# Performance work log

Hardware: AMD Instinct MI355X
Metric: run time of the kernel (lower is better)

Reference implementation:

```python
import jax, jax.numpy as jnp
import numpy as np

EPS = 1e-5
LEAK = 0.1
NPOINT = 4096
NSAMPLE = 32


def setup_inputs() -> dict:
    key = jax.random.key(0)
    ks = jax.random.split(key, 6)
    B, N, Cin = 2, 16384, 64
    ch = [Cin + 3, 64, 64, 128]
    xyz = jax.random.normal(ks[0], (B, 3, N), jnp.float32)
    points = jax.random.normal(ks[1], (B, Cin, N), jnp.float32)
    W0 = jax.random.normal(ks[2], (ch[1], ch[0]), jnp.float32) * 0.05
    W1 = jax.random.normal(ks[3], (ch[2], ch[1]), jnp.float32) * 0.05
    W2 = jax.random.normal(ks[4], (ch[3], ch[2]), jnp.float32) * 0.05
    return dict(
        xyz=xyz, points=points, W0=W0, W1=W1, W2=W2,
        g0=jnp.ones((ch[1],), jnp.float32), b0=jnp.zeros((ch[1],), jnp.float32),
        g1=jnp.ones((ch[2],), jnp.float32), b1=jnp.zeros((ch[2],), jnp.float32),
        g2=jnp.ones((ch[3],), jnp.float32), b2=jnp.zeros((ch[3],), jnp.float32),
    )


def _mlp_bn_act(x, W, g, b):
    # 1x1 conv (no bias) + BatchNorm2d (training: batch stats, biased var) + LeakyReLU(0.1)
    x = jnp.einsum('oc,bcsk->bosk', W, x)
    m = jnp.mean(x, axis=(0, 2, 3), keepdims=True)
    v = jnp.mean(jnp.square(x - m), axis=(0, 2, 3), keepdims=True)
    x = (x - m) * jax.lax.rsqrt(v + EPS) * g[None, :, None, None] + b[None, :, None, None]
    return jnp.where(x >= 0, x, LEAK * x)


def reference(xyz, points, W0, W1, W2, g0, b0, g1, b1, g2, b2):
    B, _, N = xyz.shape
    xyz_t = jnp.transpose(xyz, (0, 2, 1))            # [B,N,3]
    new_xyz = xyz[:, :, :NPOINT]                     # [B,3,S]  (use_fps=False path)
    new_xyz_t = jnp.transpose(new_xyz, (0, 2, 1))    # [B,S,3]

    # squared distances [B,S,N]
    d = (jnp.sum(new_xyz_t ** 2, -1)[:, :, None]
         + jnp.sum(xyz_t ** 2, -1)[:, None, :]
         - 2.0 * jnp.einsum('bsc,bnc->bsn', new_xyz_t, xyz_t))
    _, knn_idx = jax.lax.top_k(-d, NSAMPLE)          # [B,S,K] nearest neighbors

    gather = jax.vmap(lambda arr, idx: arr[idx])     # ([N,C],[S,K]) -> [S,K,C]
    neighbor_xyz = gather(xyz_t, knn_idx)            # [B,S,K,3]
    direction = neighbor_xyz - new_xyz_t[:, :, None, :]
    grouped = gather(jnp.transpose(points, (0, 2, 1)), knn_idx)  # [B,S,K,Cin]

    x = jnp.transpose(jnp.concatenate([direction, grouped], -1), (0, 3, 1, 2))  # [B,Cin+3,S,K]
    x = _mlp_bn_act(x, W0, g0, b0)
    x = _mlp_bn_act(x, W1, g1, b1)
    x = _mlp_bn_act(x, W2, g2, b2)
    new_points = jnp.max(x, axis=-1)                 # [B,128,S] max-pool over nsample
    return new_xyz, new_points
```

## Files before the change

kernel.cpp:

```cpp
#include <hip/hip_runtime.h>
#include <hip/hip_bf16.h>
#include <stdint.h>

#define N_ALL   16384
#define NPOINT  4096
#define KNN_K   32
#define BATCH   2
#define P_TOT   (BATCH*NPOINT*KNN_K)
#define P_TOTF  262144.0f
#define EPSV    1e-5f

typedef __attribute__((ext_vector_type(8))) short bf16x8;
typedef __attribute__((ext_vector_type(4))) float f32x4;

__device__ unsigned short g_knn[P_TOT];
__device__ __attribute__((aligned(16))) float g_pxyzn[BATCH*N_ALL*4];
__device__ __attribute__((aligned(16))) short g_ptb[BATCH*N_ALL*64];
__device__ __attribute__((aligned(16))) short g_x0b[(size_t)P_TOT*64];
__device__ __attribute__((aligned(16))) short g_x1b[(size_t)P_TOT*64];
__device__ __attribute__((aligned(16))) float g_mx[(size_t)BATCH*NPOINT*128];
__device__ __attribute__((aligned(16))) float g_mn[(size_t)BATCH*NPOINT*128];
__device__ __attribute__((aligned(16))) short g_Wb0[4*3*64*8];
__device__ __attribute__((aligned(16))) short g_Wb1[4*2*64*8];
__device__ __attribute__((aligned(16))) short g_Wb2[8*2*64*8];
__device__ float g_p0s[4][128];
__device__ float g_p1s[4][128];
__device__ float g_p2s[8][256];

__device__ __forceinline__ float b2f(short s) {
  union { unsigned u; float f; } v; v.u = ((unsigned)(unsigned short)s) << 16; return v.f;
}
__device__ __forceinline__ short f2b(float f) {
  union { float f; unsigned u; } v; v.f = f;
  unsigned u = v.u;
  u += 0x7FFFu + ((u >> 16) & 1u);
  return (short)(u >> 16);
}
__device__ __forceinline__ unsigned pkbf(float a, float b) {
  union { __hip_bfloat162 h; unsigned u; } v;
  v.h = __float22bfloat162_rn(make_float2(a, b));
  return v.u;
}
__device__ __forceinline__ unsigned long long bperm64(unsigned long long v, int byteaddr) {
  int lo = __builtin_amdgcn_ds_bpermute(byteaddr, (int)(unsigned)(v & 0xFFFFFFFFULL));
  int hi = __builtin_amdgcn_ds_bpermute(byteaddr, (int)(unsigned)(v >> 32));
  return (((unsigned long long)(unsigned)hi) << 32) | (unsigned)lo;
}
__device__ __forceinline__ unsigned long long u64min(unsigned long long a, unsigned long long b) {
  return a < b ? a : b;
}
__device__ __forceinline__ unsigned long long selstage(unsigned long long v,
                                                       unsigned long long pv, bool mx) {
  bool lt = v < pv;
  return (lt != mx) ? v : pv;
}

__device__ __forceinline__ void knn_merge32(unsigned long long& vL,
                                            unsigned long long& worst,
                                            unsigned& worst_hi, float& wd,
                                            unsigned long long vB, int hl,
                                            int aX1, int aX2, int aX4, int aX8,
                                            int aX16, int aRev, int aW) {
  vB = selstage(vB, bperm64(vB, aX1),  ((hl & 1) != 0) != ((hl & 2) != 0));
  vB = selstage(vB, bperm64(vB, aX2),  ((hl & 2) != 0) != ((hl & 4) != 0));
  vB = selstage(vB, bperm64(vB, aX1),  ((hl & 1) != 0) != ((hl & 4) != 0));
  vB = selstage(vB, bperm64(vB, aX4),  ((hl & 4) != 0) != ((hl & 8) != 0));
  vB = selstage(vB, bperm64(vB, aX2),  ((hl & 2) != 0) != ((hl & 8) != 0));
  vB = selstage(vB, bperm64(vB, aX1),  ((hl & 1) != 0) != ((hl & 8) != 0));
  vB = selstage(vB, bperm64(vB, aX8),  ((hl & 8) != 0) != ((hl & 16) != 0));
  vB = selstage(vB, bperm64(vB, aX4),  ((hl & 4) != 0) != ((hl & 16) != 0));
  vB = selstage(vB, bperm64(vB, aX2),  ((hl & 2) != 0) != ((hl & 16) != 0));
  vB = selstage(vB, bperm64(vB, aX1),  ((hl & 1) != 0) != ((hl & 16) != 0));
  vB = selstage(vB, bperm64(vB, aX16), (hl & 16) != 0);
  vB = selstage(vB, bperm64(vB, aX8),  (hl & 8) != 0);
  vB = selstage(vB, bperm64(vB, aX4),  (hl & 4) != 0);
  vB = selstage(vB, bperm64(vB, aX2),  (hl & 2) != 0);
  vB = selstage(vB, bperm64(vB, aX1),  (hl & 1) != 0);
  vL = u64min(vL, bperm64(vB, aRev));
  vL = selstage(vL, bperm64(vL, aX16), (hl & 16) != 0);
  vL = selstage(vL, bperm64(vL, aX8),  (hl & 8) != 0);
  vL = selstage(vL, bperm64(vL, aX4),  (hl & 4) != 0);
  vL = selstage(vL, bperm64(vL, aX2),  (hl & 2) != 0);
  vL = selstage(vL, bperm64(vL, aX1),  (hl & 1) != 0);
  worst = bperm64(vL, aW);
  worst_hi = (unsigned)(worst >> 32);
  unsigned wh = worst_hi;
  unsigned ub = (wh & 0x80000000u) ? (wh ^ 0x80000000u) : ~wh;
  wd = (wh == 0xFFFFFFFFu) ? __builtin_inff() : __uint_as_float(ub);
}

__global__ __launch_bounds__(256) void k_setup(const float* __restrict__ xyz,
                                               const float* __restrict__ points,
                                               const float* __restrict__ W0,
                                               const float* __restrict__ W1,
                                               const float* __restrict__ W2,
                                               float* __restrict__ out) {
#pragma clang fp contract(off)
  __shared__ float tile[64][65];
  int blk = blockIdx.x;
  int t = threadIdx.x;
  if (blk < 512) {
    int b  = blk >> 8;
    int n0 = (blk & 255) << 6;
#pragma unroll
    for (int r = 0; r < 16; r++) {
      int lin = r * 256 + t;
      int c = lin >> 6, nn = lin & 63;
      tile[c][nn] = points[((size_t)(b * 64 + c)) * N_ALL + n0 + nn];
    }
    __syncthreads();
#pragma unroll
    for (int r = 0; r < 16; r++) {
      int lin = r * 256 + t;
      int nn = lin >> 6, c = lin & 63;
      g_ptb[((size_t)(b * N_ALL + n0 + nn)) * 64 + c] = f2b(tile[c][nn]);
    }
  } else if (blk < 640) {
    int i = (blk - 512) * 256 + t;
    if (i < 24576) {
      int s = i & 4095;
      int c = (i >> 12) % 3;
      int b = i / 12288;
      out[i] = xyz[(b * 3 + c) * N_ALL + s];
    }
    int b = i >> 14, n = i & 16383;
    const float* xb = xyz + b * 3 * N_ALL;
    float x = xb[n], y = xb[N_ALL + n], z = xb[2 * N_ALL + n];
    float4 p; p.x = x; p.y = y; p.z = z; p.w = x * x + y * y + z * z;
    ((float4*)g_pxyzn)[i] = p;
  } else {
    for (int i = t; i < 4 * 3 * 64 * 8; i += 256) {
      int j = i & 7, lane = (i >> 3) & 63, rest = i >> 9;
      int kt = rest % 3, mt = rest / 3;
      int m = 16 * mt + (lane & 15);
      int k = 32 * kt + (lane >> 4) * 8 + j;
      float v = 0.f;
      if (k < 64) v = W0[m * 67 + 3 + k];
      else if (k < 67) v = W0[m * 67 + (k - 64)];
      g_Wb0[i] = f2b(v);
    }
    for (int i = t; i < 4 * 2 * 64 * 8; i += 256) {
      int j = i & 7, lane = (i >> 3) & 63;
      int kt = (i >> 9) & 1, mt = i >> 10;
      int m = 16 * mt + (lane & 15);
      int k = 32 * kt + (lane >> 4) * 8 + j;
      g_Wb1[i] = f2b(W1[m * 64 + k]);
    }
    for (int i = t; i < 8 * 2 * 64 * 8; i += 256) {
      int j = i & 7, lane = (i >> 3) & 63;
      int kt = (i >> 9) & 1, mt = i >> 10;
      int m = 16 * mt + (lane & 15);
      int k = 32 * kt + (lane >> 4) * 8 + j;
      g_Wb2[i] = f2b(W2[m * 64 + k]);
    }
    float* z0 = &g_p0s[0][0];
    float* z1 = &g_p1s[0][0];
    float* z2 = &g_p2s[0][0];
    for (int i = t; i < 512; i += 256) { z0[i] = 0.f; z1[i] = 0.f; }
    for (int i = t; i < 2048; i += 256) z2[i] = 0.f;
  }
}

__global__ __launch_bounds__(256, 8) void k_knn() {
#pragma clang fp contract(off)
  __shared__ unsigned long long buf[4][2][64];
  int wv = threadIdx.x >> 6;
  int lane = threadIdx.x & 63;
  int half = lane >> 5;
  int hl = lane & 31;
  int lanebase = lane & 32;
  unsigned long long* bufh = buf[wv][half];

  int qpair = wv >> 1;
  int range = wv & 1;
  int q = blockIdx.x * 4 + qpair * 2 + half;
  int b = q >> 12, s = q & 4095;
  const float4* pb = (const float4*)g_pxyzn + (b << 14);
  float4 qp = pb[s];
  float qx = qp.x, qy = qp.y, qz = qp.z, qn = qp.w;

  int aX1  = (lanebase | (hl ^ 1))  << 2;
  int aX2  = (lanebase | (hl ^ 2))  << 2;
  int aX4  = (lanebase | (hl ^ 4))  << 2;
  int aX8  = (lanebase | (hl ^ 8))  << 2;
  int aX16 = (lanebase | (hl ^ 16)) << 2;
  int aRev = (lanebase | (31 - hl)) << 2;
  int aW   = (lanebase | 31)        << 2;

  unsigned long long vL = ~0ULL;
  unsigned long long worst = ~0ULL;
  unsigned worst_hi = 0xFFFFFFFFu;
  float wd = __builtin_inff();
  int F = 0;

  int base = range << 13;
  for (int n0 = base; n0 < base + 8192; n0 += 128) {
    float4 p0 = pb[n0 + hl];
    float4 p1 = pb[n0 + 32 + hl];
    float4 p2 = pb[n0 + 64 + hl];
    float4 p3 = pb[n0 + 96 + hl];
    float d[4];
    {
      float dt0 = (qx * p0.x + qy * p0.y) + qz * p0.z;
      float dt1 = (qx * p1.x + qy * p1.y) + qz * p1.z;
      float dt2 = (qx * p2.x + qy * p2.y) + qz * p2.z;
      float dt3 = (qx * p3.x + qy * p3.y) + qz * p3.z;
      d[0] = __builtin_fmaf(-2.0f, dt0, qn + p0.w);
      d[1] = __builtin_fmaf(-2.0f, dt1, qn + p1.w);
      d[2] = __builtin_fmaf(-2.0f, dt2, qn + p2.w);
      d[3] = __builtin_fmaf(-2.0f, dt3, qn + p3.w);
    }
    float md = fminf(fminf(d[0], d[1]), fminf(d[2], d[3]));
    if (__ballot(md <= wd)) {
#pragma unroll
      for (int t = 0; t < 4; t++) {
        bool sv = d[t] <= wd;
        unsigned long long bl = __ballot(sv);
        unsigned mb = half ? (unsigned)(bl >> 32) : (unsigned)bl;
        if (sv) {
          unsigned u = __float_as_uint(d[t]);
          u ^= ((unsigned)(((int)u) >> 31)) | 0x80000000u;
          unsigned long long c = (((unsigned long long)u) << 32)
                               | (unsigned)(n0 + 32 * t + hl);
          bufh[F + __popc(mb & ((1u << hl) - 1u))] = c;
        }
        F += __popc(mb);
        if (__ballot(F >= 32)) {
          int take = F >= 32 ? 32 : F;
          unsigned long long vB = (hl < take) ? bufh[hl] : ~0ULL;
          knn_merge32(vL, worst, worst_hi, wd, vB, hl,
                      aX1, aX2, aX4, aX8, aX16, aRev, aW);
          int R = F - take;
          if (hl < R) bufh[hl] = bufh[32 + hl];
          F = R;
        }
      }
    }
  }
  if (__ballot(F > 0)) {
    unsigned long long vB = (hl < F) ? bufh[hl] : ~0ULL;
    knn_merge32(vL, worst, worst_hi, wd, vB, hl, aX1, aX2, aX4, aX8, aX16, aRev, aW);
  }

  bufh[hl] = vL;
  __syncthreads();
  unsigned long long vB = buf[wv ^ 1][half][hl];
  vL = u64min(vL, bperm64(vB, aRev));
  vL = selstage(vL, bperm64(vL, aX16), (hl & 16) != 0);
  vL = selstage(vL, bperm64(vL, aX8),  (hl & 8) != 0);
  vL = selstage(vL, bperm64(vL, aX4),  (hl & 4) != 0);
  vL = selstage(vL, bperm64(vL, aX2),  (hl & 2) != 0);
  vL = selstage(vL, bperm64(vL, aX1),  (hl & 1) != 0);
  if (range == 0)
    g_knn[((size_t)q << 5) | hl] = (unsigned short)(vL & 0xFFFF);
}

__global__ __launch_bounds__(256) void k_l0(const float* __restrict__ xyz) {
  __shared__ __attribute__((aligned(16))) short feats[256][104];
  int t = threadIdx.x;
  int p0 = blockIdx.x * 256;
  {
    int p = p0 + t;
    int idx = g_knn[p];
    int s = (p >> 5) & 4095;
    int b = p >> 17;
    const short* src = g_ptb + ((size_t)((b << 14) + idx) << 6);
#pragma unroll
    for (int i = 0; i < 8; i++)
      ((int4*)&feats[t][0])[i] = ((const int4*)src)[i];
    const float* xb = xyz + b * 3 * N_ALL;
    int4 z; z.x = 0; z.y = 0; z.z = 0; z.w = 0;
    *(int4*)&feats[t][64] = z;
    *(int4*)&feats[t][72] = z;
    *(int4*)&feats[t][80] = z;
    *(int4*)&feats[t][88] = z;
    short4 d3;
    d3.x = f2b(xb[idx] - xb[s]);
    d3.y = f2b(xb[N_ALL + idx] - xb[N_ALL + s]);
    d3.z = f2b(xb[2 * N_ALL + idx] - xb[2 * N_ALL + s]);
    d3.w = 0;
    *(short4*)&feats[t][64] = d3;
  }
  __syncthreads();
  int lane = t & 63, wv = t >> 6;
  int l15 = lane & 15, quad = lane >> 4;
  bf16x8 A[4][3];
#pragma unroll
  for (int mt = 0; mt < 4; mt++)
#pragma unroll
    for (int kt = 0; kt < 3; kt++)
      A[mt][kt] = *(const bf16x8*)(g_Wb0 + (((mt * 3 + kt) * 64 + lane) << 3));
  f32x4 C[4][4];
#pragma unroll
  for (int mt = 0; mt < 4; mt++)
#pragma unroll
    for (int nt = 0; nt < 4; nt++) C[mt][nt] = 0.f;
#pragma unroll
  for (int kt = 0; kt < 3; kt++)
#pragma unroll
    for (int nt = 0; nt < 4; nt++) {
      bf16x8 B = *(const bf16x8*)(&feats[wv * 64 + nt * 16 + l15][kt * 32 + quad * 8]);
#pragma unroll
      for (int mt = 0; mt < 4; mt++)
        C[mt][nt] = __builtin_amdgcn_mfma_f32_16x16x32_bf16(A[mt][kt], B, C[mt][nt], 0, 0, 0);
    }
  float sA[16], qA[16];
#pragma unroll
  for (int i = 0; i < 16; i++) { sA[i] = 0.f; qA[i] = 0.f; }
#pragma unroll
  for (int mt = 0; mt < 4; mt++)
#pragma unroll
    for (int nt = 0; nt < 4; nt++) {
      int p = p0 + wv * 64 + nt * 16 + l15;
      int c0 = mt * 16 + quad * 4;
      uint2 o;
      o.x = pkbf(C[mt][nt][0], C[mt][nt][1]);
      o.y = pkbf(C[mt][nt][2], C[mt][nt][3]);
      *(uint2*)(g_x0b + ((size_t)p << 6) + c0) = o;
      float v0 = __uint_as_float(o.x << 16);
      float v1 = __uint_as_float(o.x & 0xFFFF0000u);
      float v2 = __uint_as_float(o.y << 16);
      float v3 = __uint_as_float(o.y & 0xFFFF0000u);
      int ib = mt * 4;
      sA[ib+0] += v0; qA[ib+0] = fmaf(v0, v0, qA[ib+0]);
      sA[ib+1] += v1; qA[ib+1] = fmaf(v1, v1, qA[ib+1]);
      sA[ib+2] += v2; qA[ib+2] = fmaf(v2, v2, qA[ib+2]);
      sA[ib+3] += v3; qA[ib+3] = fmaf(v3, v3, qA[ib+3]);
    }
  __syncthreads();
  float* red = (float*)&feats[0][0];
  int rb = t * 36;
#pragma unroll
  for (int w = 0; w < 4; w++) {
    float4 vs; vs.x = sA[w*4+0]; vs.y = sA[w*4+1]; vs.z = sA[w*4+2]; vs.w = sA[w*4+3];
    float4 vq; vq.x = qA[w*4+0]; vq.y = qA[w*4+1]; vq.z = qA[w*4+2]; vq.w = qA[w*4+3];
    *(float4*)&red[rb + w*4] = vs;
    *(float4*)&red[rb + 16 + w*4] = vq;
  }
  __syncthreads();
  if (t < 64) {
    int qd = (t >> 2) & 3;
    int i = ((t >> 4) << 2) | (t & 3);
    float S = 0.f, Q = 0.f;
#pragma unroll
    for (int w = 0; w < 4; w++)
#pragma unroll
      for (int l = 0; l < 16; l++) {
        int row = (w * 64 + qd * 16 + l) * 36;
        S += red[row + i];
        Q += red[row + 16 + i];
      }
    float* sh = &g_p0s[blockIdx.x & 3][0];
    atomicAdd(sh + t, S);
    atomicAdd(sh + 64 + t, Q);
  }
}

__global__ __launch_bounds__(256) void k_l1(const float* __restrict__ g0,
                                            const float* __restrict__ b0) {
  __shared__ float scA[64], shA[64];
  __shared__ __attribute__((aligned(16))) float red[256 * 36];
  int t = threadIdx.x;
  if (t < 64) {
    float ps = g_p0s[0][t] + g_p0s[1][t] + g_p0s[2][t] + g_p0s[3][t];
    float pq = g_p0s[0][64+t] + g_p0s[1][64+t] + g_p0s[2][64+t] + g_p0s[3][64+t];
    float m = ps / P_TOTF;
    float v = pq / P_TOTF - m * m;
    float sc = g0[t] / sqrtf(v + EPSV);
    scA[t] = sc; shA[t] = b0[t] - m * sc;
  }
  __syncthreads();
  int lane = t & 63, wv = t >> 6;
  int l15 = lane & 15, quad = lane >> 4;
  int p0 = blockIdx.x * 256 + wv * 64;
  float scv[2][8], shv[2][8];
#pragma unroll
  for (int kt = 0; kt < 2; kt++)
#pragma unroll
    for (int j = 0; j < 8; j++) {
      int c = kt * 32 + quad * 8 + j;
      scv[kt][j] = scA[c]; shv[kt][j] = shA[c];
    }
  bf16x8 A[4][2];
#pragma unroll
  for (int mt = 0; mt < 4; mt++)
#pragma unroll
    for (int kt = 0; kt < 2; kt++)
      A[mt][kt] = *(const bf16x8*)(g_Wb1 + (((mt * 2 + kt) * 64 + lane) << 3));
  f32x4 C[4][4];
#pragma unroll
  for (int mt = 0; mt < 4; mt++)
#pragma unroll
    for (int nt = 0; nt < 4; nt++) C[mt][nt] = 0.f;
#pragma unroll
  for (int kt = 0; kt < 2; kt++)
#pragma unroll
    for (int nt = 0; nt < 4; nt++) {
      const short* src = g_x0b + (((size_t)(p0 + nt * 16 + l15)) << 6) + kt * 32 + quad * 8;
      uint4 raw = *(const uint4*)src;
      bf16x8 B;
      unsigned* Bu = (unsigned*)&B;
      unsigned ru[4] = {raw.x, raw.y, raw.z, raw.w};
#pragma unroll
      for (int jj = 0; jj < 4; jj++) {
        float lo = __uint_as_float(ru[jj] << 16);
        float hi = __uint_as_float(ru[jj] & 0xFFFF0000u);
        float a0 = lo * scv[kt][2*jj]   + shv[kt][2*jj];
        float a1 = hi * scv[kt][2*jj+1] + shv[kt][2*jj+1];
        a0 = fmaxf(a0, 0.1f * a0);
        a1 = fmaxf(a1, 0.1f * a1);
        Bu[jj] = pkbf(a0, a1);
      }
#pragma unroll
      for (int mt = 0; mt < 4; mt++)
        C[mt][nt] = __builtin_amdgcn_mfma_f32_16x16x32_bf16(A[mt][kt], B, C[mt][nt], 0, 0, 0);
    }
  float sA[16], qA[16];
#pragma unroll
  for (int i = 0; i < 16; i++) { sA[i] = 0.f; qA[i] = 0.f; }
#pragma unroll
  for (int mt = 0; mt < 4; mt++)
#pragma unroll
    for (int nt = 0; nt < 4; nt++) {
      int p = p0 + nt * 16 + l15;
      int c0 = mt * 16 + quad * 4;
      uint2 o;
      o.x = pkbf(C[mt][nt][0], C[mt][nt][1]);
      o.y = pkbf(C[mt][nt][2], C[mt][nt][3]);
      *(uint2*)(g_x1b + ((size_t)p << 6) + c0) = o;
      float v0 = __uint_as_float(o.x << 16);
      float v1 = __uint_as_float(o.x & 0xFFFF0000u);
      float v2 = __uint_as_float(o.y << 16);
      float v3 = __uint_as_float(o.y & 0xFFFF0000u);
      int ib = mt * 4;
      sA[ib+0] += v0; qA[ib+0] = fmaf(v0, v0, qA[ib+0]);
      sA[ib+1] += v1; qA[ib+1] = fmaf(v1, v1, qA[ib+1]);
      sA[ib+2] += v2; qA[ib+2] = fmaf(v2, v2, qA[ib+2]);
      sA[ib+3] += v3; qA[ib+3] = fmaf(v3, v3, qA[ib+3]);
    }
  int rb = t * 36;
#pragma unroll
  for (int w = 0; w < 4; w++) {
    float4 vs; vs.x = sA[w*4+0]; vs.y = sA[w*4+1]; vs.z = sA[w*4+2]; vs.w = sA[w*4+3];
    float4 vq; vq.x = qA[w*4+0]; vq.y = qA[w*4+1]; vq.z = qA[w*4+2]; vq.w = qA[w*4+3];
    *(float4*)&red[rb + w*4] = vs;
    *(float4*)&red[rb + 16 + w*4] = vq;
  }
  __syncthreads();
  if (t < 64) {
    int qd = (t >> 2) & 3;
    int i = ((t >> 4) << 2) | (t & 3);
    float S = 0.f, Q = 0.f;
#pragma unroll
    for (int w = 0; w < 4; w++)
#pragma unroll
      for (int l = 0; l < 16; l++) {
        int row = (w * 64 + qd * 16 + l) * 36;
        S += red[row + i];
        Q += red[row + 16 + i];
      }
    float* sh = &g_p1s[blockIdx.x & 3][0];
    atomicAdd(sh + t, S);
    atomicAdd(sh + 64 + t, Q);
  }
}

__global__ __launch_bounds__(256) void k_l2(const float* __restrict__ g1,
                                            const float* __restrict__ b1) {
  __shared__ float scA[64], shA[64];
  __shared__ __attribute__((aligned(16))) float red[9216];
  int t = threadIdx.x;
  if (t < 64) {
    float ps = g_p1s[0][t] + g_p1s[1][t] + g_p1s[2][t] + g_p1s[3][t];
    float pq = g_p1s[0][64+t] + g_p1s[1][64+t] + g_p1s[2][64+t] + g_p1s[3][64+t];
    float m = ps / P_TOTF;
    float v = pq / P_TOTF - m * m;
    float sc = g1[t] / sqrtf(v + EPSV);
    scA[t] = sc; shA[t] = b1[t] - m * sc;
  }
  __syncthreads();
  int lane = t & 63, wv = t >> 6;
  int l15 = lane & 15, quad = lane >> 4;
  int chh = wv & 1;
  int p0 = blockIdx.x * 128 + (wv >> 1) * 64;
  float scv[2][8], shv[2][8];
#pragma unroll
  for (int kt = 0; kt < 2; kt++)
#pragma unroll
    for (int j = 0; j < 8; j++) {
      int c = kt * 32 + quad * 8 + j;
      scv[kt][j] = scA[c]; shv[kt][j] = shA[c];
    }
  bf16x8 A[4][2];
#pragma unroll
  for (int mt = 0; mt < 4; mt++)
#pragma unroll
    for (int kt = 0; kt < 2; kt++)
      A[mt][kt] = *(const bf16x8*)(g_Wb2 + ((((4 * chh + mt) * 2 + kt) * 64 + lane) << 3));
  f32x4 C[4][4];
#pragma unroll
  for (int mt = 0; mt < 4; mt++)
#pragma unroll
    for (int nt = 0; nt < 4; nt++) C[mt][nt] = 0.f;
#pragma unroll
  for (int kt = 0; kt < 2; kt++)
#pragma unroll
    for (int nt = 0; nt < 4; nt++) {
      const short* src = g_x1b + (((size_t)(p0 + nt * 16 + l15)) << 6) + kt * 32 + quad * 8;
      uint4 raw = *(const uint4*)src;
      bf16x8 B;
      unsigned* Bu = (unsigned*)&B;
      unsigned ru[4] = {raw.x, raw.y, raw.z, raw.w};
#pragma unroll
      for (int jj = 0; jj < 4; jj++) {
        float lo = __uint_as_float(ru[jj] << 16);
        float hi = __uint_as_float(ru[jj] & 0xFFFF0000u);
        float a0 = lo * scv[kt][2*jj]   + shv[kt][2*jj];
        float a1 = hi * scv[kt][2*jj+1] + shv[kt][2*jj+1];
        a0 = fmaxf(a0, 0.1f * a0);
        a1 = fmaxf(a1, 0.1f * a1);
        Bu[jj] = pkbf(a0, a1);
      }
#pragma unroll
      for (int mt = 0; mt < 4; mt++)
        C[mt][nt] = __builtin_amdgcn_mfma_f32_16x16x32_bf16(A[mt][kt], B, C[mt][nt], 0, 0, 0);
    }
  float sA[16], qA[16];
  float mxP[2][16], mnP[2][16];
#pragma unroll
  for (int i = 0; i < 16; i++) {
    sA[i] = 0.f; qA[i] = 0.f;
    mxP[0][i] = -3.4e38f; mnP[0][i] = 3.4e38f;
    mxP[1][i] = -3.4e38f; mnP[1][i] = 3.4e38f;
  }
#pragma unroll
  for (int mt = 0; mt < 4; mt++)
#pragma unroll
    for (int nt = 0; nt < 4; nt++) {
      unsigned ox = pkbf(C[mt][nt][0], C[mt][nt][1]);
      unsigned oy = pkbf(C[mt][nt][2], C[mt][nt][3]);
      float v0 = __uint_as_float(ox << 16);
      float v1 = __uint_as_float(ox & 0xFFFF0000u);
      float v2 = __uint_as_float(oy << 16);
      float v3 = __uint_as_float(oy & 0xFFFF0000u);
      int ib = mt * 4, sp = nt >> 1;
      sA[ib+0] += v0; qA[ib+0] = fmaf(v0, v0, qA[ib+0]);
      sA[ib+1] += v1; qA[ib+1] = fmaf(v1, v1, qA[ib+1]);
      sA[ib+2] += v2; qA[ib+2] = fmaf(v2, v2, qA[ib+2]);
      sA[ib+3] += v3; qA[ib+3] = fmaf(v3, v3, qA[ib+3]);
      mxP[sp][ib+0] = fmaxf(mxP[sp][ib+0], v0); mnP[sp][ib+0] = fminf(mnP[sp][ib+0], v0);
      mxP[sp][ib+1] = fmaxf(mxP[sp][ib+1], v1); mnP[sp][ib+1] = fminf(mnP[sp][ib+1], v1);
      mxP[sp][ib+2] = fmaxf(mxP[sp][ib+2], v2); mnP[sp][ib+2] = fminf(mnP[sp][ib+2], v2);
      mxP[sp][ib+3] = fmaxf(mxP[sp][ib+3], v3); mnP[sp][ib+3] = fminf(mnP[sp][ib+3], v3);
    }
  short* mxs = (short*)red;
  short* mns = mxs + 8448;
  int sgl0 = (wv >> 1) * 2;
#pragma unroll
  for (int sp = 0; sp < 2; sp++)
#pragma unroll
    for (int mt = 0; mt < 4; mt++) {
      int c0 = (4 * chh + mt) * 16 + quad * 4;
      int base = ((sgl0 + sp) * 16 + l15) * 132 + c0;
      short4 m4;
      m4.x = f2b(mxP[sp][mt*4+0]); m4.y = f2b(mxP[sp][mt*4+1]);
      m4.z = f2b(mxP[sp][mt*4+2]); m4.w = f2b(mxP[sp][mt*4+3]);
      *(short4*)&mxs[base] = m4;
      short4 n4;
      n4.x = f2b(mnP[sp][mt*4+0]); n4.y = f2b(mnP[sp][mt*4+1]);
      n4.z = f2b(mnP[sp][mt*4+2]); n4.w = f2b(mnP[sp][mt*4+3]);
      *(short4*)&mns[base] = n4;
    }
  __syncthreads();
  {
    int sg = t >> 6, c0 = (t & 63) * 2;
    float m0 = -3.4e38f, m1 = -3.4e38f, n0 = 3.4e38f, n1 = 3.4e38f;
#pragma unroll
    for (int l = 0; l < 16; l++) {
      unsigned ux = *(const unsigned*)&mxs[(sg * 16 + l) * 132 + c0];
      m0 = fmaxf(m0, __uint_as_float(ux << 16));
      m1 = fmaxf(m1, __uint_as_float(ux & 0xFFFF0000u));
      unsigned un = *(const unsigned*)&mns[(sg * 16 + l) * 132 + c0];
      n0 = fminf(n0, __uint_as_float(un << 16));
      n1 = fminf(n1, __uint_as_float(un & 0xFFFF0000u));
    }
    int sgg = blockIdx.x * 4 + sg;
    float2 vmx; vmx.x = m0; vmx.y = m1;
    float2 vmn; vmn.x = n0; vmn.y = n1;
    *(float2*)(g_mx + ((size_t)sgg << 7) + c0) = vmx;
    *(float2*)(g_mn + ((size_t)sgg << 7) + c0) = vmn;
  }
  __syncthreads();
  int rb = t * 36;
#pragma unroll
  for (int w = 0; w < 4; w++) {
    float4 vs; vs.x = sA[w*4+0]; vs.y = sA[w*4+1]; vs.z = sA[w*4+2]; vs.w = sA[w*4+3];
    float4 vq; vq.x = qA[w*4+0]; vq.y = qA[w*4+1]; vq.z = qA[w*4+2]; vq.w = qA[w*4+3];
    *(float4*)&red[rb + w*4] = vs;
    *(float4*)&red[rb + 16 + w*4] = vq;
  }
  __syncthreads();
  if (t < 128) {
    int c = t;
    int ch2 = c >> 6, mt = (c >> 4) & 3, qd = (c >> 2) & 3, j = c & 3;
    int i = mt * 4 + j;
    float S = 0.f, Q = 0.f;
#pragma unroll
    for (int w = 0; w < 2; w++) {
      int wvv = ch2 + w * 2;
#pragma unroll
      for (int l = 0; l < 16; l++) {
        int row = (wvv * 64 + qd * 16 + l) * 36;
        S += red[row + i];
        Q += red[row + 16 + i];
      }
    }
    float* sh = &g_p2s[blockIdx.x & 7][0];
    atomicAdd(sh + c, S);
    atomicAdd(sh + 128 + c, Q);
  }
}

__global__ __launch_bounds__(256) void k_epi(const float* __restrict__ g2,
                                             const float* __restrict__ b2,
                                             float* __restrict__ out) {
  __shared__ float scA[128], shA[128];
  __shared__ float res[16][132];
  int t = threadIdx.x;
  if (t < 128) {
    float ps = 0.f, pq = 0.f;
#pragma unroll
    for (int s = 0; s < 8; s++) { ps += g_p2s[s][t]; pq += g_p2s[s][128 + t]; }
    float m = ps / P_TOTF;
    float v = pq / P_TOTF - m * m;
    float sc = g2[t] / sqrtf(v + EPSV);
    scA[t] = sc; shA[t] = b2[t] - m * sc;
  }
  __syncthreads();
  int cp = t & 63, sl = t >> 6;
  int c0 = cp * 2, c1 = c0 + 1;
  float sc0 = scA[c0], sh0 = shA[c0];
  float sc1 = scA[c1], sh1 = shA[c1];
  int sg0 = blockIdx.x * 16;
  for (int it = 0; it < 4; it++) {
    int sgl = sl * 4 + it;
    size_t off = ((size_t)(sg0 + sgl) << 7) + c0;
    float2 vmx = *(const float2*)(g_mx + off);
    float2 vmn = *(const float2*)(g_mn + off);
    float a0 = (sc0 >= 0.f ? vmx.x : vmn.x) * sc0 + sh0; a0 = fmaxf(a0, 0.1f * a0);
    float a1 = (sc1 >= 0.f ? vmx.y : vmn.y) * sc1 + sh1; a1 = fmaxf(a1, 0.1f * a1);
    res[sgl][c0] = a0; res[sgl][c1] = a1;
  }
  __syncthreads();
  int b = sg0 >> 12, s0 = sg0 & 4095;
#pragma unroll
  for (int w = 0; w < 2; w++) {
    int fidx = t * 2 + w;
    int c = fidx >> 2, qi = fidx & 3;
    float4 o;
    o.x = res[qi * 4 + 0][c];
    o.y = res[qi * 4 + 1][c];
    o.z = res[qi * 4 + 2][c];
    o.w = res[qi * 4 + 3][c];
    *(float4*)(out + 24576 + (((size_t)(b * 128 + c)) << 12) + s0 + qi * 4) = o;
  }
}

extern "C" void kernel_launch(void* const* d_in, const int* in_sizes, int n_in,
                              void* d_out, int out_size, void* d_ws, size_t ws_size,
                              hipStream_t stream) {
  (void)in_sizes; (void)n_in; (void)out_size; (void)d_ws; (void)ws_size;
  const float* xyz    = (const float*)d_in[0];
  const float* points = (const float*)d_in[1];
  const float* W0     = (const float*)d_in[2];
  const float* W1     = (const float*)d_in[3];
  const float* W2     = (const float*)d_in[4];
  const float* g0     = (const float*)d_in[5];
  const float* b0     = (const float*)d_in[6];
  const float* g1     = (const float*)d_in[7];
  const float* b1     = (const float*)d_in[8];
  const float* g2     = (const float*)d_in[9];
  const float* b2     = (const float*)d_in[10];
  float* out = (float*)d_out;

  hipLaunchKernelGGL(k_setup, dim3(641),  dim3(256), 0, stream, xyz, points, W0, W1, W2, out);
  hipLaunchKernelGGL(k_knn,   dim3(2048), dim3(256), 0, stream);
  hipLaunchKernelGGL(k_l0,    dim3(1024), dim3(256), 0, stream, xyz);
  hipLaunchKernelGGL(k_l1,    dim3(1024), dim3(256), 0, stream, g0, b0);
  hipLaunchKernelGGL(k_l2,    dim3(2048), dim3(256), 0, stream, g1, b1);
  hipLaunchKernelGGL(k_epi,   dim3(512),  dim3(256), 0, stream, g2, b2, out);
}
```

Baseline: 289.9 us.

## Halve k_l0 tile to 128 points with split-thread gathers and smaller LDS reduction

k_l0 now handles 128 points per block, so twice as many blocks are launched. Two threads share each point's 64-channel feature gather, and the xyz offset is read as one float4 from the packed g_pxyzn array instead of six scalar loads from xyz. The reduction scratch shrinks from 36 to 20 floats per thread, so the sum and sum-of-squares passes now run one after the other. Together these cut LDS and register use per block to raise occupancy, at the cost of extra barriers and more partial-stat slots (8 instead of 4).

Result: no change. 284.6 us (-1.8%).

```diff
diff --git a/kernel.cpp b/kernel.cpp
--- a/kernel.cpp
+++ b/kernel.cpp
@@ -23,7 +23,7 @@
 __device__ __attribute__((aligned(16))) short g_Wb0[4*3*64*8];
 __device__ __attribute__((aligned(16))) short g_Wb1[4*2*64*8];
 __device__ __attribute__((aligned(16))) short g_Wb2[8*2*64*8];
-__device__ float g_p0s[4][128];
+__device__ float g_p0s[8][128];
 __device__ float g_p1s[4][128];
 __device__ float g_p2s[8][256];
 
@@ -156,7 +156,8 @@
     float* z0 = &g_p0s[0][0];
     float* z1 = &g_p1s[0][0];
     float* z2 = &g_p2s[0][0];
-    for (int i = t; i < 512; i += 256) { z0[i] = 0.f; z1[i] = 0.f; }
+    for (int i = t; i < 1024; i += 256) z0[i] = 0.f;
+    for (int i = t; i < 512; i += 256) z1[i] = 0.f;
     for (int i = t; i < 2048; i += 256) z2[i] = 0.f;
   }
 }
@@ -255,31 +256,37 @@
     g_knn[((size_t)q << 5) | hl] = (unsigned short)(vL & 0xFFFF);
 }
 
-__global__ __launch_bounds__(256) void k_l0(const float* __restrict__ xyz) {
-  __shared__ __attribute__((aligned(16))) short feats[256][104];
+__global__ __launch_bounds__(256) void k_l0() {
+  __shared__ __attribute__((aligned(16))) short feats[128][104];
   int t = threadIdx.x;
-  int p0 = blockIdx.x * 256;
+  int p0 = blockIdx.x * 128;
   {
-    int p = p0 + t;
+    int pt = t >> 1, h = t & 1;
+    int p = p0 + pt;
     int idx = g_knn[p];
     int s = (p >> 5) & 4095;
     int b = p >> 17;
-    const short* src = g_ptb + ((size_t)((b << 14) + idx) << 6);
-#pragma unroll
-    for (int i = 0; i < 8; i++)
-      ((int4*)&feats[t][0])[i] = ((const int4*)src)[i];
-    const float* xb = xyz + b * 3 * N_ALL;
-    int4 z; z.x = 0; z.y = 0; z.z = 0; z.w = 0;
-    *(int4*)&feats[t][64] = z;
-    *(int4*)&feats[t][72] = z;
-    *(int4*)&feats[t][80] = z;
-    *(int4*)&feats[t][88] = z;
-    short4 d3;
-    d3.x = f2b(xb[idx] - xb[s]);
-    d3.y = f2b(xb[N_ALL + idx] - xb[N_ALL + s]);
-    d3.z = f2b(xb[2 * N_ALL + idx] - xb[2 * N_ALL + s]);
-    d3.w = 0;
-    *(short4*)&feats[t][64] = d3;
+    const short* src = g_ptb + ((size_t)((b << 14) + idx) << 6) + h * 32;
+#pragma unroll
+    for (int i = 0; i < 4; i++)
+      ((int4*)&feats[pt][h * 32])[i] = ((const int4*)src)[i];
+    if (h == 0) {
+      const float4* pb4 = (const float4*)g_pxyzn + (b << 14);
+      float4 a = pb4[idx], q = pb4[s];
+      short4 d3;
+      d3.x = f2b(a.x - q.x);
+      d3.y = f2b(a.y - q.y);
+      d3.z = f2b(a.z - q.z);
+      d3.w = 0;
+      *(short4*)&feats[pt][64] = d3;
+      short4 z4; z4.x = 0; z4.y = 0; z4.z = 0; z4.w = 0;
+      *(short4*)&feats[pt][68] = z4;
+    } else {
+      int4 z; z.x = 0; z.y = 0; z.z = 0; z.w = 0;
+      *(int4*)&feats[pt][72] = z;
+      *(int4*)&feats[pt][80] = z;
+      *(int4*)&feats[pt][88] = z;
+    }
   }
   __syncthreads();
   int lane = t & 63, wv = t >> 6;
@@ -290,16 +297,16 @@
 #pragma unroll
     for (int kt = 0; kt < 3; kt++)
       A[mt][kt] = *(const bf16x8*)(g_Wb0 + (((mt * 3 + kt) * 64 + lane) << 3));
-  f32x4 C[4][4];
-#pragma unroll
-  for (int mt = 0; mt < 4; mt++)
-#pragma unroll
-    for (int nt = 0; nt < 4; nt++) C[mt][nt] = 0.f;
+  f32x4 C[4][2];
+#pragma unroll
+  for (int mt = 0; mt < 4; mt++)
+#pragma unroll
+    for (int nt = 0; nt < 2; nt++) C[mt][nt] = 0.f;
 #pragma unroll
   for (int kt = 0; kt < 3; kt++)
 #pragma unroll
-    for (int nt = 0; nt < 4; nt++) {
-      bf16x8 B = *(const bf16x8*)(&feats[wv * 64 + nt * 16 + l15][kt * 32 + quad * 8]);
+    for (int nt = 0; nt < 2; nt++) {
+      bf16x8 B = *(const bf16x8*)(&feats[wv * 32 + nt * 16 + l15][kt * 32 + quad * 8]);
 #pragma unroll
       for (int mt = 0; mt < 4; mt++)
         C[mt][nt] = __builtin_amdgcn_mfma_f32_16x16x32_bf16(A[mt][kt], B, C[mt][nt], 0, 0, 0);
@@ -310,8 +317,8 @@
 #pragma unroll
   for (int mt = 0; mt < 4; mt++)
 #pragma unroll
-    for (int nt = 0; nt < 4; nt++) {
-      int p = p0 + wv * 64 + nt * 16 + l15;
+    for (int nt = 0; nt < 2; nt++) {
+      int p = p0 + wv * 32 + nt * 16 + l15;
       int c0 = mt * 16 + quad * 4;
       uint2 o;
       o.x = pkbf(C[mt][nt][0], C[mt][nt][1]);
@@ -329,29 +336,41 @@
     }
   __syncthreads();
   float* red = (float*)&feats[0][0];
-  int rb = t * 36;
+  int rb = t * 20;
 #pragma unroll
   for (int w = 0; w < 4; w++) {
     float4 vs; vs.x = sA[w*4+0]; vs.y = sA[w*4+1]; vs.z = sA[w*4+2]; vs.w = sA[w*4+3];
-    float4 vq; vq.x = qA[w*4+0]; vq.y = qA[w*4+1]; vq.z = qA[w*4+2]; vq.w = qA[w*4+3];
     *(float4*)&red[rb + w*4] = vs;
-    *(float4*)&red[rb + 16 + w*4] = vq;
-  }
-  __syncthreads();
+  }
+  __syncthreads();
+  float* sh = &g_p0s[blockIdx.x & 7][0];
   if (t < 64) {
     int qd = (t >> 2) & 3;
     int i = ((t >> 4) << 2) | (t & 3);
-    float S = 0.f, Q = 0.f;
+    float S = 0.f;
 #pragma unroll
     for (int w = 0; w < 4; w++)
 #pragma unroll
-      for (int l = 0; l < 16; l++) {
-        int row = (w * 64 + qd * 16 + l) * 36;
-        S += red[row + i];
-        Q += red[row + 16 + i];
-      }
-    float* sh = &g_p0s[blockIdx.x & 3][0];
+      for (int l = 0; l < 16; l++)
+        S += red[(w * 64 + qd * 16 + l) * 20 + i];
     atomicAdd(sh + t, S);
+  }
+  __syncthreads();
+#pragma unroll
+  for (int w = 0; w < 4; w++) {
+    float4 vq; vq.x = qA[w*4+0]; vq.y = qA[w*4+1]; vq.z = qA[w*4+2]; vq.w = qA[w*4+3];
+    *(float4*)&red[rb + w*4] = vq;
+  }
+  __syncthreads();
+  if (t < 64) {
+    int qd = (t >> 2) & 3;
+    int i = ((t >> 4) << 2) | (t & 3);
+    float Q = 0.f;
+#pragma unroll
+    for (int w = 0; w < 4; w++)
+#pragma unroll
+      for (int l = 0; l < 16; l++)
+        Q += red[(w * 64 + qd * 16 + l) * 20 + i];
     atomicAdd(sh + 64 + t, Q);
   }
 }
@@ -362,8 +381,9 @@
   __shared__ __attribute__((aligned(16))) float red[256 * 36];
   int t = threadIdx.x;
   if (t < 64) {
-    float ps = g_p0s[0][t] + g_p0s[1][t] + g_p0s[2][t] + g_p0s[3][t];
-    float pq = g_p0s[0][64+t] + g_p0s[1][64+t] + g_p0s[2][64+t] + g_p0s[3][64+t];
+    float ps = 0.f, pq = 0.f;
+#pragma unroll
+    for (int s = 0; s < 8; s++) { ps += g_p0s[s][t]; pq += g_p0s[s][64 + t]; }
     float m = ps / P_TOTF;
     float v = pq / P_TOTF - m * m;
     float sc = g0[t] / sqrtf(v + EPSV);
@@ -685,7 +705,7 @@
 
   hipLaunchKernelGGL(k_setup, dim3(641),  dim3(256), 0, stream, xyz, points, W0, W1, W2, out);
   hipLaunchKernelGGL(k_knn,   dim3(2048), dim3(256), 0, stream);
-  hipLaunchKernelGGL(k_l0,    dim3(1024), dim3(256), 0, stream, xyz);
+  hipLaunchKernelGGL(k_l0,    dim3(2048), dim3(256), 0, stream);
   hipLaunchKernelGGL(k_l1,    dim3(1024), dim3(256), 0, stream, g0, b0);
   hipLaunchKernelGGL(k_l2,    dim3(2048), dim3(256), 0, stream, g1, b1);
   hipLaunchKernelGGL(k_epi,   dim3(512),  dim3(256), 0, stream, g2, b2, out);
```
